# Kernel optimization log

Measured on AMD Instinct MI355X. Metric: run time of the kernel, lower is better.

Reference implementation:

```python
import jax, jax.numpy as jnp
import numpy as np

B, S, K, N, GROUPS, GS = 4, 2048, 4096, 4096, 32, 128


def setup_inputs() -> dict:
    key = jax.random.key(0)
    k1, k2, k3, k4, k5 = jax.random.split(key, 5)
    x = jax.random.normal(k1, (B, S, K), dtype=jnp.float32)
    # int8-stored quantized weights in [-128, 127], layout [K, N] (in_features, out_features)
    weight_int8 = jax.random.randint(k2, (K, N), -128, 128, dtype=jnp.int32)
    # per-group, per-output-column positive scales
    scales = (jax.random.uniform(k3, (GROUPS, N), dtype=jnp.float32) * 0.01 + 1e-4)
    bias = jax.random.normal(k4, (N,), dtype=jnp.float32) * 0.02
    # column reordering permutation (high-sensitivity cols first in the real module)
    col_indices = jax.random.permutation(k5, K).astype(jnp.int32)
    return {"x": x, "scales": scales, "bias": bias,
            "weight_int8": weight_int8, "col_indices": col_indices,
            "group_size": GS}


def reference(x, scales, bias, weight_int8, col_indices, group_size):
    orig_shape = x.shape
    k = x.shape[-1]
    x2 = x.reshape(-1, k)                      # [M, K]
    # CPR column reordering of the activations (weights are stored pre-reordered)
    x_reordered = x2[:, col_indices]           # [M, K]
    # per-group dequant: scale row-group g applies to rows [g*gs, (g+1)*gs) of W
    s_full = jnp.repeat(scales, group_size, axis=0)[:k]          # [K, N]
    w_deq = weight_int8.astype(x.dtype) * s_full                 # [K, N]
    y = x_reordered @ w_deq + bias                               # [M, N]
    return y.reshape(*orig_shape[:-1], y.shape[-1])
```

## Files before the change

### kernel.cpp

```cpp
#include <hip/hip_runtime.h>
#include <hip/hip_bf16.h>

#define M_DIM 8192
#define N_DIM 4096
#define K_DIM 4096
#define NT (K_DIM / 32)

typedef __bf16 bf16x8 __attribute__((ext_vector_type(8)));
typedef float f32x4 __attribute__((ext_vector_type(4)));
typedef unsigned short ushort8v __attribute__((ext_vector_type(8)));

typedef const __attribute__((address_space(1))) void gv_t;
typedef __attribute__((address_space(3))) void lv_t;

static __device__ __forceinline__ unsigned short f2bf(float f) {
  unsigned u = __builtin_bit_cast(unsigned, f);
  u += 0x7fffu + ((u >> 16) & 1u);
  return (unsigned short)(u >> 16);
}

__global__ void k_pinv(const int* __restrict__ ci, int* __restrict__ pinv) {
  int k = blockIdx.x * 256 + threadIdx.x;
  if (k < K_DIM) pinv[ci[k]] = k;
}

__global__ void k_cvt(const float* __restrict__ x, unsigned short* __restrict__ xb) {
  const long n4 = (long)M_DIM * K_DIM / 4;
  for (long i = (long)blockIdx.x * 256 + threadIdx.x; i < n4; i += 2048L * 256) {
    float4 v = *(const float4*)(x + i * 4);
    ushort4 o;
    o.x = f2bf(v.x); o.y = f2bf(v.y); o.z = f2bf(v.z); o.w = f2bf(v.w);
    *(ushort4*)(xb + i * 4) = o;
  }
}

__global__ void k_w2t(const int* __restrict__ w, const float* __restrict__ scales,
                      const int* __restrict__ pinv, unsigned short* __restrict__ w2t) {
  __shared__ int tile[64 * 68];
  __shared__ int grp[64];
  __shared__ int krow[64];
  const int n0 = blockIdx.x * 64;
  const int c0 = blockIdx.y * 64;
  const int t = threadIdx.x;
  if (t < 64) {
    int kk = pinv[c0 + t];
    krow[t] = kk;
    grp[t] = kk >> 7;
  }
  __syncthreads();
  {
    const int ci = t >> 2, q = t & 3;
    const int kk = krow[ci];
    const int* src = w + (long)kk * N_DIM + n0 + q * 16;
#pragma unroll
    for (int j = 0; j < 4; ++j) {
      int4 v = *(const int4*)(src + j * 4);
      *(int4*)&tile[ci * 68 + q * 16 + j * 4] = v;
    }
  }
  __syncthreads();
  {
    const int nj = t >> 2, cq = t & 3;
    const int n = n0 + nj;
    unsigned short outv[16];
#pragma unroll
    for (int i = 0; i < 16; ++i) {
      int cii = cq * 16 + i;
      float f = (float)tile[cii * 68 + nj] * scales[grp[cii] * N_DIM + n];
      outv[i] = f2bf(f);
    }
    unsigned short* dst = w2t + (long)n * K_DIM + c0 + cq * 16;
    *(ushort8v*)(dst)     = *(ushort8v*)&outv[0];
    *(ushort8v*)(dst + 8) = *(ushort8v*)&outv[8];
  }
}

__global__ __launch_bounds__(512, 2) void k_gemm(const unsigned short* __restrict__ A,
                                                 const unsigned short* __restrict__ Bt,
                                                 const float* __restrict__ bias,
                                                 float* __restrict__ C) {
  __shared__ __attribute__((aligned(16))) char lds[3 * 32768];

  const int bid = blockIdx.x;
  const int swz = (bid & 7) * 64 + (bid >> 3);
  const int by = swz >> 4;
  const int bx = swz & 15;

  const int tid = threadIdx.x;
  const int l = tid & 63;
  const int w = tid >> 6;
  const int wr = w >> 2;
  const int wc = w & 3;
  const int r4 = l & 15;
  const int kb = (l >> 4) << 4;
  const int rmask = (r4 & 14) << 3;

  const int wmask = ((tid >> 3) & 7) << 4;
  const char* srcA[2];
  const char* srcB[2];
  {
    const char* Ab = (const char*)A + (size_t)(by * 256) * (K_DIM * 2);
    const char* Bb = (const char*)Bt + (size_t)(bx * 256) * (K_DIM * 2);
#pragma unroll
    for (int j = 0; j < 2; ++j) {
      int L = j * 8192 + tid * 16;
      int lg = L ^ wmask;
      int row = lg >> 6, kbo = lg & 63;
      srcA[j] = Ab + (size_t)row * (K_DIM * 2) + kbo;
      srcB[j] = Bb + (size_t)row * (K_DIM * 2) + kbo;
    }
  }
  const int stgoff = tid * 16;

  const int aoff = (((wr * 128 + r4) << 6) + kb) ^ rmask;
  const int boff = (((wc * 64  + r4) << 6) + kb) ^ rmask;

  f32x4 acc[8][4];
  const f32x4 z = {0.f, 0.f, 0.f, 0.f};
#pragma unroll
  for (int mi = 0; mi < 8; ++mi)
#pragma unroll
    for (int ni = 0; ni < 4; ++ni) acc[mi][ni] = z;

#pragma unroll
  for (int tt = 0; tt < 2; ++tt) {
    char* ab = lds + tt * 32768;
    char* bb = ab + 16384;
#pragma unroll
    for (int j = 0; j < 2; ++j) {
      __builtin_amdgcn_global_load_lds((gv_t*)(srcA[j] + tt * 64), (lv_t*)(ab + j * 8192 + stgoff), 16, 0, 0);
      __builtin_amdgcn_global_load_lds((gv_t*)(srcB[j] + tt * 64), (lv_t*)(bb + j * 8192 + stgoff), 16, 0, 0);
    }
  }
  asm volatile("s_waitcnt vmcnt(4)" ::: "memory");
  __builtin_amdgcn_sched_barrier(0);
  __builtin_amdgcn_s_barrier();
  __builtin_amdgcn_sched_barrier(0);

  int cur = 0;
  for (int t = 0; t < NT; ++t) {
    char* ab = lds + cur * 32768;
    char* bb = ab + 16384;
    int stg = cur + 2; if (stg >= 3) stg -= 3;
    char* sab = lds + stg * 32768;
    char* sbb = sab + 16384;
    const bool pf = (t + 2 < NT);
    const long koff = (long)(t + 2) * 64;

    bf16x8 af[4], bf[4];
#pragma unroll
    for (int mi = 0; mi < 4; ++mi)
      af[mi] = *(const bf16x8*)(ab + aoff + mi * 1024);
#pragma unroll
    for (int ni = 0; ni < 4; ++ni)
      bf[ni] = *(const bf16x8*)(bb + boff + ni * 1024);
    if (pf) {
      __builtin_amdgcn_global_load_lds((gv_t*)(srcA[0] + koff), (lv_t*)(sab + stgoff), 16, 0, 0);
      __builtin_amdgcn_global_load_lds((gv_t*)(srcA[1] + koff), (lv_t*)(sab + 8192 + stgoff), 16, 0, 0);
    }
    __builtin_amdgcn_sched_barrier(0);
    __builtin_amdgcn_s_barrier();
    __builtin_amdgcn_sched_barrier(0);
    __builtin_amdgcn_s_setprio(1);
#pragma unroll
    for (int mi = 0; mi < 4; ++mi)
#pragma unroll
      for (int ni = 0; ni < 4; ++ni)
        acc[mi][ni] = __builtin_amdgcn_mfma_f32_16x16x32_bf16(af[mi], bf[ni], acc[mi][ni], 0, 0, 0);
    __builtin_amdgcn_s_setprio(0);
    __builtin_amdgcn_sched_barrier(0);
    __builtin_amdgcn_s_barrier();
    __builtin_amdgcn_sched_barrier(0);

#pragma unroll
    for (int mi = 0; mi < 4; ++mi)
      af[mi] = *(const bf16x8*)(ab + aoff + 4096 + mi * 1024);
    if (pf) {
      __builtin_amdgcn_global_load_lds((gv_t*)(srcB[0] + koff), (lv_t*)(sbb + stgoff), 16, 0, 0);
      __builtin_amdgcn_global_load_lds((gv_t*)(srcB[1] + koff), (lv_t*)(sbb + 8192 + stgoff), 16, 0, 0);
    }
    __builtin_amdgcn_sched_barrier(0);
    __builtin_amdgcn_s_barrier();
    __builtin_amdgcn_sched_barrier(0);
    __builtin_amdgcn_s_setprio(1);
#pragma unroll
    for (int mi = 0; mi < 4; ++mi)
#pragma unroll
      for (int ni = 0; ni < 4; ++ni)
        acc[4 + mi][ni] = __builtin_amdgcn_mfma_f32_16x16x32_bf16(af[mi], bf[ni], acc[4 + mi][ni], 0, 0, 0);
    __builtin_amdgcn_s_setprio(0);
    if (t < NT - 2)       asm volatile("s_waitcnt vmcnt(4)" ::: "memory");
    else if (t == NT - 2) asm volatile("s_waitcnt vmcnt(0)" ::: "memory");
    __builtin_amdgcn_sched_barrier(0);
    __builtin_amdgcn_s_barrier();
    __builtin_amdgcn_sched_barrier(0);

    cur = (cur == 2) ? 0 : cur + 1;
  }

  const int row0 = by * 256 + wr * 128 + ((l >> 4) << 2);
  const int col0 = bx * 256 + wc * 64 + r4;
#pragma unroll
  for (int ni = 0; ni < 4; ++ni) {
    const int col = col0 + ni * 16;
    const float bv = bias[col];
#pragma unroll
    for (int mi = 0; mi < 8; ++mi) {
#pragma unroll
      for (int r = 0; r < 4; ++r)
        C[(size_t)(row0 + mi * 16 + r) * N_DIM + col] = acc[mi][ni][r] + bv;
    }
  }
}

__global__ void k_fallback(const float* __restrict__ x, const float* __restrict__ scales,
                           const float* __restrict__ bias, const int* __restrict__ w,
                           const int* __restrict__ ci, float* __restrict__ out) {
  const int n = blockIdx.x * 256 + threadIdx.x;
  const int m0 = blockIdx.y * 32;
  float acc[32];
#pragma unroll
  for (int i = 0; i < 32; ++i) acc[i] = 0.f;
  for (int k = 0; k < K_DIM; ++k) {
    int c = ci[k];
    float wv = (float)w[(long)k * N_DIM + n] * scales[(k >> 7) * N_DIM + n];
#pragma unroll 8
    for (int mm = 0; mm < 32; ++mm)
      acc[mm] += x[(long)(m0 + mm) * K_DIM + c] * wv;
  }
  float bv = bias[n];
  for (int mm = 0; mm < 32; ++mm)
    out[(long)(m0 + mm) * N_DIM + n] = acc[mm] + bv;
}

extern "C" void kernel_launch(void* const* d_in, const int* in_sizes, int n_in,
                              void* d_out, int out_size, void* d_ws, size_t ws_size,
                              hipStream_t stream) {
  const float* x      = (const float*)d_in[0];
  const float* scales = (const float*)d_in[1];
  const float* bias   = (const float*)d_in[2];
  const int*   wq     = (const int*)d_in[3];
  const int*   ci     = (const int*)d_in[4];
  float* out = (float*)d_out;

  const size_t xb_bytes  = (size_t)M_DIM * K_DIM * 2;
  const size_t w2t_bytes = (size_t)N_DIM * K_DIM * 2;
  const size_t need = xb_bytes + w2t_bytes + (size_t)K_DIM * 4;

  if (ws_size < need) {
    k_fallback<<<dim3(N_DIM / 256, M_DIM / 32), 256, 0, stream>>>(x, scales, bias, wq, ci, out);
    return;
  }

  unsigned short* xb  = (unsigned short*)d_ws;
  unsigned short* w2t = (unsigned short*)((char*)d_ws + xb_bytes);
  int* pinv           = (int*)((char*)d_ws + xb_bytes + w2t_bytes);

  k_pinv<<<K_DIM / 256, 256, 0, stream>>>(ci, pinv);
  k_cvt<<<2048, 256, 0, stream>>>(x, xb);
  k_w2t<<<dim3(N_DIM / 64, K_DIM / 64), 256, 0, stream>>>(wq, scales, pinv, w2t);
  k_gemm<<<(M_DIM / 256) * (N_DIM / 256), 512, 0, stream>>>(xb, w2t, bias, out);
}
```

Measured before the change: 324.1 us.

## Software-pipeline LDS fragment loads across K iterations to overlap with MFMA

Restructures the main K loop so the A and B register fragments for the next tile are read from LDS during the current tile's MFMA phases. The first-half A/B fragments are preloaded before the loop, and the second-half A fragment is loaded ahead of the first MFMA block. The vmcnt wait and barriers are moved so LDS reads no longer sit on the critical path before each MFMA group. This aims to hide LDS latency behind matrix math, at the cost of more live registers and a tighter ordering between the global-to-LDS prefetch waits and the next-buffer reads.

```diff
diff --git a/kernel.cpp b/kernel.cpp
--- a/kernel.cpp
+++ b/kernel.cpp
@@ -127,15 +127,22 @@
     char* ab = lds + tt * 32768;
     char* bb = ab + 16384;
 #pragma unroll
-    for (int j = 0; j < 2; ++j) {
+    for (int j = 0; j < 2; ++j)
       __builtin_amdgcn_global_load_lds((gv_t*)(srcA[j] + tt * 64), (lv_t*)(ab + j * 8192 + stgoff), 16, 0, 0);
+#pragma unroll
+    for (int j = 0; j < 2; ++j)
       __builtin_amdgcn_global_load_lds((gv_t*)(srcB[j] + tt * 64), (lv_t*)(bb + j * 8192 + stgoff), 16, 0, 0);
-    }
   }
   asm volatile("s_waitcnt vmcnt(4)" ::: "memory");
   __builtin_amdgcn_sched_barrier(0);
   __builtin_amdgcn_s_barrier();
   __builtin_amdgcn_sched_barrier(0);
+
+  bf16x8 fA[4], fB[4], gA1[4];
+#pragma unroll
+  for (int mi = 0; mi < 4; ++mi) fA[mi] = *(const bf16x8*)(lds + aoff + mi * 1024);
+#pragma unroll
+  for (int ni = 0; ni < 4; ++ni) fB[ni] = *(const bf16x8*)(lds + 16384 + boff + ni * 1024);
 
   int cur = 0;
   for (int t = 0; t < NT; ++t) {
@@ -144,58 +151,61 @@
     int stg = cur + 2; if (stg >= 3) stg -= 3;
     char* sab = lds + stg * 32768;
     char* sbb = sab + 16384;
-    const bool pf = (t + 2 < NT);
+    int nxt = cur + 1; if (nxt >= 3) nxt -= 3;
+    char* nab = lds + nxt * 32768;
+    char* nbb = nab + 16384;
     const long koff = (long)(t + 2) * 64;
 
-    bf16x8 af[4], bf[4];
-#pragma unroll
-    for (int mi = 0; mi < 4; ++mi)
-      af[mi] = *(const bf16x8*)(ab + aoff + mi * 1024);
-#pragma unroll
-    for (int ni = 0; ni < 4; ++ni)
-      bf[ni] = *(const bf16x8*)(bb + boff + ni * 1024);
-    if (pf) {
+    if (t + 2 < NT) {
       __builtin_amdgcn_global_load_lds((gv_t*)(srcA[0] + koff), (lv_t*)(sab + stgoff), 16, 0, 0);
       __builtin_amdgcn_global_load_lds((gv_t*)(srcA[1] + koff), (lv_t*)(sab + 8192 + stgoff), 16, 0, 0);
     }
+#pragma unroll
+    for (int mi = 0; mi < 4; ++mi)
+      gA1[mi] = *(const bf16x8*)(ab + aoff + 4096 + mi * 1024);
+
+    __builtin_amdgcn_s_setprio(1);
+#pragma unroll
+    for (int mi = 0; mi < 4; ++mi)
+#pragma unroll
+      for (int ni = 0; ni < 4; ++ni)
+        acc[mi][ni] = __builtin_amdgcn_mfma_f32_16x16x32_bf16(fA[mi], fB[ni], acc[mi][ni], 0, 0, 0);
+    __builtin_amdgcn_s_setprio(0);
+
+    if (t < NT - 2)       asm volatile("s_waitcnt vmcnt(2)" ::: "memory");
+    else if (t == NT - 2) asm volatile("s_waitcnt vmcnt(0)" ::: "memory");
     __builtin_amdgcn_sched_barrier(0);
     __builtin_amdgcn_s_barrier();
     __builtin_amdgcn_sched_barrier(0);
-    __builtin_amdgcn_s_setprio(1);
-#pragma unroll
-    for (int mi = 0; mi < 4; ++mi)
-#pragma unroll
-      for (int ni = 0; ni < 4; ++ni)
-        acc[mi][ni] = __builtin_amdgcn_mfma_f32_16x16x32_bf16(af[mi], bf[ni], acc[mi][ni], 0, 0, 0);
-    __builtin_amdgcn_s_setprio(0);
-    __builtin_amdgcn_sched_barrier(0);
-    __builtin_amdgcn_s_barrier();
-    __builtin_amdgcn_sched_barrier(0);
-
-#pragma unroll
-    for (int mi = 0; mi < 4; ++mi)
-      af[mi] = *(const bf16x8*)(ab + aoff + 4096 + mi * 1024);
-    if (pf) {
+
+    if (t + 2 < NT) {
       __builtin_amdgcn_global_load_lds((gv_t*)(srcB[0] + koff), (lv_t*)(sbb + stgoff), 16, 0, 0);
       __builtin_amdgcn_global_load_lds((gv_t*)(srcB[1] + koff), (lv_t*)(sbb + 8192 + stgoff), 16, 0, 0);
     }
+    if (t + 1 < NT) {
+#pragma unroll
+      for (int mi = 0; mi < 4; ++mi)
+        fA[mi] = *(const bf16x8*)(nab + aoff + mi * 1024);
+    }
+
+    __builtin_amdgcn_s_setprio(1);
+#pragma unroll
+    for (int mi = 0; mi < 4; ++mi)
+#pragma unroll
+      for (int ni = 0; ni < 4; ++ni)
+        acc[4 + mi][ni] = __builtin_amdgcn_mfma_f32_16x16x32_bf16(gA1[mi], fB[ni], acc[4 + mi][ni], 0, 0, 0);
+    __builtin_amdgcn_s_setprio(0);
+
+    if (t + 1 < NT) {
+#pragma unroll
+      for (int ni = 0; ni < 4; ++ni)
+        fB[ni] = *(const bf16x8*)(nbb + boff + ni * 1024);
+    }
     __builtin_amdgcn_sched_barrier(0);
     __builtin_amdgcn_s_barrier();
     __builtin_amdgcn_sched_barrier(0);
-    __builtin_amdgcn_s_setprio(1);
-#pragma unroll
-    for (int mi = 0; mi < 4; ++mi)
-#pragma unroll
-      for (int ni = 0; ni < 4; ++ni)
-        acc[4 + mi][ni] = __builtin_amdgcn_mfma_f32_16x16x32_bf16(af[mi], bf[ni], acc[4 + mi][ni], 0, 0, 0);
-    __builtin_amdgcn_s_setprio(0);
-    if (t < NT - 2)       asm volatile("s_waitcnt vmcnt(4)" ::: "memory");
-    else if (t == NT - 2) asm volatile("s_waitcnt vmcnt(0)" ::: "memory");
-    __builtin_amdgcn_sched_barrier(0);
-    __builtin_amdgcn_s_barrier();
-    __builtin_amdgcn_sched_barrier(0);
-
-    cur = (cur == 2) ? 0 : cur + 1;
+
+    cur = nxt;
   }
 
   const int row0 = by * 256 + wr * 128 + ((l >> 4) << 2);
```

New measurement: 313.4 us. 3.3% less time.
